# Kernel optimization log

Measured on AMD Instinct MI355X. Metric: run time of the kernel, lower is better.

## Reference

```python
import jax, jax.numpy as jnp
import numpy as np
from jax import lax

TS = 64.0  # timestep_ in the original module


def get_spikes(x, th):
    # Integrate-and-fire with reset-by-subtraction (catCuda.getSpikes),
    # batched over all channels with per-channel thresholds.
    # x: [N,C,H,W,T], th: [C]
    thb = th[None, :, None, None]
    xT = jnp.moveaxis(x, -1, 0)  # [T,N,C,H,W]

    def step(v, xt):
        v = v + xt
        s = (v >= thb).astype(x.dtype)
        return v - s * thb, s

    _, sT = lax.scan(step, jnp.zeros_like(xT[0]), xT)
    return jnp.moveaxis(sT, 0, -1)  # [N,C,H,W,T]


def conv2d(x, w, b, pad):
    out = lax.conv_general_dilated(x, w, (1, 1), [(pad, pad), (pad, pad)],
                                   dimension_numbers=('NCHW', 'OIHW', 'NCHW'))
    return out + b[None, :, None, None]


def snn_conv(x, w, b, pad):
    # per-timestep 2D conv on [N,C,H,W,T]: fold T into batch
    N, C, H, W, T = x.shape
    xt = jnp.moveaxis(x, -1, 1).reshape(N * T, C, H, W)
    out = conv2d(xt, w, b, pad)
    Co, Ho, Wo = out.shape[1], out.shape[2], out.shape[3]
    return jnp.moveaxis(out.reshape(N, T, Co, Ho, Wo), 1, -1)


def avgpool2(y):
    N, C, H, W = y.shape
    return y.reshape(N, C, H // 2, 2, W // 2, 2).mean(axis=(3, 5))


def snn_pool(x):
    N, C, H, W, T = x.shape
    return x.reshape(N, C, H // 2, 2, W // 2, 2, T).mean(axis=(3, 5))


def tt(x5, y4, th):
    # threshold_training_snn: spikes from SNN pre-activation, quantized-clamped
    # ANN activation, and online per-channel threshold update.
    y_new = get_spikes(x5, th)
    y = jnp.clip(jnp.floor(y4 * TS) / TS, 0.0, 1.0)
    mul = x5.shape[0] * x5.shape[2] * x5.shape[3] * x5.shape[4]
    diff = (y.sum(axis=(0, 2, 3)) * TS - y_new.sum(axis=(0, 2, 3, 4))) / mul
    return y_new, y, th - 0.1 * diff


def setup_inputs():
    key = jax.random.key(0)
    ks = jax.random.split(key, 40)
    chans = [(3, 128), (128, 128), (128, 256), (256, 256), (256, 512), (512, 512), (512, 1024)]
    inp = {}
    for idx, (ci, co) in enumerate(chans):
        inp['w%ds' % (idx + 1)] = jax.random.normal(ks[2 * idx], (co, ci, 3, 3), jnp.float32) / np.float32(np.sqrt(ci * 9))
        inp['b%ds' % (idx + 1)] = jnp.zeros((co,), jnp.float32)
        inp['w%da' % (idx + 1)] = jax.random.normal(ks[2 * idx + 1], (co, ci, 3, 3), jnp.float32) / np.float32(np.sqrt(ci * 9))
        inp['b%da' % (idx + 1)] = jnp.zeros((co,), jnp.float32)
    inp['wc'] = jax.random.normal(ks[30], (100, 1024), jnp.float32) / 32.0
    inp['bc'] = jnp.zeros((100,), jnp.float32)
    inp['x'] = jax.random.uniform(ks[31], (4, 3, 32, 32, 64), jnp.float32)
    for name, c in [('threshold_pre_1', 128), ('threshold_pre_2', 128), ('threshold_pre_3', 256),
                    ('threshold_pre_4', 256), ('threshold_pre_5', 512), ('threshold_pre_6', 512),
                    ('threshold_pre_7', 1024), ('p1', 128), ('p2', 256), ('p3', 512), ('p4', 1024)]:
        inp[name] = jnp.ones((c,), jnp.float32)
    return inp


def reference(x, threshold_pre_1, threshold_pre_2, threshold_pre_3, threshold_pre_4,
              threshold_pre_5, threshold_pre_6, threshold_pre_7, p1, p2, p3, p4,
              w1s, b1s, w1a, b1a, w2s, b2s, w2a, b2a, w3s, b3s, w3a, b3a,
              w4s, b4s, w4a, b4a, w5s, b5s, w5a, b5a, w6s, b6s, w6a, b6a,
              w7s, b7s, w7a, b7a, wc, bc):
    x_ = x.sum(axis=-1) / TS
    xs, y, t1 = tt(snn_conv(x, w1s, b1s, 1), conv2d(x_, w1a, b1a, 1), threshold_pre_1)
    xs, y, t2 = tt(snn_conv(xs, w2s, b2s, 1), conv2d(y, w2a, b2a, 1), threshold_pre_2)
    xs, y, q1 = tt(snn_pool(xs), avgpool2(y), p1)
    xs, y, t3 = tt(snn_conv(xs, w3s, b3s, 1), conv2d(y, w3a, b3a, 1), threshold_pre_3)
    xs, y, t4 = tt(snn_conv(xs, w4s, b4s, 1), conv2d(y, w4a, b4a, 1), threshold_pre_4)
    xs, y, q2 = tt(snn_pool(xs), avgpool2(y), p2)
    xs, y, t5 = tt(snn_conv(xs, w5s, b5s, 1), conv2d(y, w5a, b5a, 1), threshold_pre_5)
    xs, y, t6 = tt(snn_conv(xs, w6s, b6s, 1), conv2d(y, w6a, b6a, 1), threshold_pre_6)
    xs, y, q3 = tt(snn_pool(xs), avgpool2(y), p3)
    xs, y, t7 = tt(snn_conv(xs, w7s, b7s, 0), conv2d(y, w7a, b7a, 0), threshold_pre_7)
    xs, y, q4 = tt(snn_pool(xs), avgpool2(y), p4)
    # classifier on [N,1024,1,1,T] spike trains, then sum over time / T
    logits_t = jnp.einsum('nct,oc->not', xs[:, :, 0, 0, :], wc) + bc[None, :, None]
    out = logits_t.sum(axis=-1) / TS
    return (out, t1, t2, t3, t4, t5, t6, t7, q1, q2, q3, q4)
```

## Files before the change

kernel.cpp:

```cpp
#include <hip/hip_runtime.h>
#include <cstdint>
#include <cstddef>


typedef short short8 __attribute__((ext_vector_type(8)));
typedef float floatx4 __attribute__((ext_vector_type(4)));

__device__ __forceinline__ unsigned short f2bf_rne(float f) {
  unsigned u = __float_as_uint(f);
  return (unsigned short)((u + 0x7FFFu + ((u >> 16) & 1u)) >> 16);
}
__device__ __forceinline__ float bf2f(unsigned short h) {
  return __uint_as_float((unsigned)h << 16);
}

__global__ __launch_bounds__(256) void k_wxform(const float* __restrict__ Wsrc,
                                                unsigned short* __restrict__ wt,
                                                int Ci, int Co) {
  const int nch = Ci >> 5;
  const int total = (Co >> 6) * nch * 9 * 4 * 64;
  int idx = blockIdx.x * 256 + threadIdx.x;
  if (idx >= total) return;
  int lane = idx & 63;
  int t2 = idx >> 6;
  int cg = t2 & 3;
  int t3 = t2 >> 2;
  int tap = t3 % 9;
  int t4 = t3 / 9;
  int ch = t4 % nch;
  int cot = t4 / nch;
  int co = cot * 64 + cg * 16 + (lane & 15);
  int cib = ch * 32 + (lane >> 4) * 8;
  short8 vh, vl;
  #pragma unroll
  for (int j = 0; j < 8; ++j) {
    float wv = Wsrc[((size_t)co * Ci + cib + j) * 9 + tap];
    unsigned short h = f2bf_rne(wv);
    vh[j] = (short)h;
    vl[j] = (short)f2bf_rne(wv - bf2f(h));
  }
  size_t base = ((((size_t)cot * nch + ch) * 9 + tap) * 4 + cg) * 1024 + (size_t)lane * 8;
  *(short8*)&wt[base] = vh;
  *(short8*)&wt[base + 512] = vl;
}

__global__ __launch_bounds__(256) void k_wxform1(const float* __restrict__ Wsrc,
                                                 unsigned short* __restrict__ wt) {
  int idx = blockIdx.x * 256 + threadIdx.x;
  if (idx >= 512) return;
  int lane = idx & 63, cg = (idx >> 6) & 3, cot = idx >> 8;
  int co = cot * 64 + cg * 16 + (lane & 15);
  short8 vh, vl;
  #pragma unroll
  for (int e = 0; e < 8; ++e) {
    int k = (lane >> 4) * 8 + e;
    float wv = 0.f;
    if (k < 27) { int tap = k / 3, ci = k - 3 * tap; wv = Wsrc[(co * 3 + ci) * 9 + tap]; }
    unsigned short h = f2bf_rne(wv);
    vh[e] = (short)h;
    vl[e] = (short)f2bf_rne(wv - bf2f(h));
  }
  size_t base = (size_t)cot * 4096 + cg * 1024 + (size_t)lane * 8;
  *(short8*)&wt[base] = vh;
  *(short8*)&wt[base + 512] = vl;
}

__global__ __launch_bounds__(256) void k_tpack(const float* __restrict__ x,
                                               unsigned* __restrict__ XT2) {
  int idx = blockIdx.x * 256 + threadIdx.x;
  int b = idx / 3072;
  int rem = idx - b * 3072;
  int t = b & 63, n = b >> 6;
  float f = x[((size_t)(n * 3072 + rem)) * 64 + t];
  unsigned short h = f2bf_rne(f);
  unsigned short l = f2bf_rne(f - bf2f(h));
  XT2[idx] = (unsigned)h | ((unsigned)l << 16);
}

__global__ __launch_bounds__(256) void k_xbar_pack(const float* __restrict__ x,
                                                   unsigned* __restrict__ xb) {
  int idx = blockIdx.x * 256 + threadIdx.x;
  if (idx >= 12288) return;
  const float* p = x + (size_t)idx * 64;
  float s = 0.f;
  #pragma unroll
  for (int t = 0; t < 64; ++t) s += p[t];
  s *= 0.015625f;
  unsigned short h = f2bf_rne(s);
  unsigned short l = f2bf_rne(s - bf2f(h));
  xb[idx] = (unsigned)h | ((unsigned)l << 16);
}

template <typename T, bool PAD0, int GW, int NPG>
__global__ __launch_bounds__(256, 1) void k_cmfma(
    const T* __restrict__ in, const unsigned short* __restrict__ wt,
    const float* __restrict__ bs, float* __restrict__ out,
    int Ci, int Co, int W, int TRI, int tpi, int NIMG, int nImgValid,
    int nchPer, size_t osplit) {
  constexpr int CW = NPG;
  constexpr int MT = 16 * GW * NPG;
  constexpr int PPXMAX = PAD0 ? (MT / 4) * 16 : 400;
  constexpr int STR = 40;
  __shared__ unsigned short sIn[PPXMAX * STR];
  const int tid = threadIdx.x;
  const int lane = tid & 63;
  const int wv = tid >> 6;
  const int cog = wv / NPG;
  const int pxg = wv % NPG;
  const int cot = blockIdx.x;
  const int mtile = blockIdx.y;
  const int kz = blockIdx.z;
  const int nch = Ci >> 5;
  const int nchA = kz * nchPer, nchB = nchA + nchPer;
  out += (size_t)kz * osplit;
  const int addBias = (kz == 0);

  int img_first, r0 = 0, PPR, PPX;
  if constexpr (PAD0) {
    img_first = mtile * (MT / 4);
    PPR = 16; PPX = (MT / 4) * 16;
  } else {
    img_first = (mtile / tpi) * NIMG;
    r0 = (mtile % tpi) * TRI;
    PPR = (TRI + 2) * (W + 2);
    PPX = NIMG * PPR;
  }
  const int TRW = TRI * W;

  int p0[GW], mimg[GW], mopx[GW];
  #pragma unroll
  for (int g = 0; g < GW; ++g) {
    int m = pxg * (GW * 16) + g * 16 + (lane & 15);
    int limg;
    if constexpr (PAD0) {
      limg = m >> 2;
      int o = m & 3;
      p0[g] = limg * 16 + (o >> 1) * 4 + (o & 1);
      mopx[g] = (o >> 1) * 2 + (o & 1);
    } else {
      limg = m / TRW;
      int rm = m - limg * TRW;
      int r = rm / W, c = rm - r * W;
      p0[g] = limg * PPR + r * (W + 2) + c;
      mopx[g] = (r0 + r) * W + c;
    }
    mimg[g] = img_first + limg;
  }
  int psh[9];
  #pragma unroll
  for (int t = 0; t < 9; ++t) {
    int dh = t / 3, dw = t - dh * 3;
    psh[t] = PAD0 ? (dh * 4 + dw) : (dh * (W + 2) + dw);
  }

  const int HWin = PAD0 ? 16 : W * W;
  int sgofs[2]; bool svalid[2];
  #pragma unroll
  for (int i = 0; i < 2; ++i) {
    int p = tid + i * 256;
    svalid[i] = false; sgofs[i] = 0;
    if (p < PPX) {
      int limg, gpx;
      if constexpr (PAD0) {
        limg = p >> 4; gpx = p & 15;
      } else {
        limg = p / PPR;
        int rem = p - limg * PPR;
        int pr = rem / (W + 2), pc = rem - pr * (W + 2);
        int gr = r0 + pr - 1, gc = pc - 1;
        gpx = (gr >= 0 && gr < W && gc >= 0 && gc < W) ? gr * W + gc : -1;
      }
      int img = img_first + limg;
      if (gpx >= 0 && img < nImgValid) {
        svalid[i] = true;
        sgofs[i] = img * Ci * HWin + gpx;
      }
    }
  }
  const int kb = (lane >> 4) * 8;

  floatx4 acc[CW][GW];
  floatx4 zero = {0.f, 0.f, 0.f, 0.f};
  #pragma unroll
  for (int cw = 0; cw < CW; ++cw)
    #pragma unroll
    for (int g = 0; g < GW; ++g) acc[cw][g] = zero;

  for (int ch = nchA; ch < nchB; ++ch) {
    const int ci0 = ch * 32;
    #pragma unroll
    for (int i = 0; i < 2; ++i) {
      int p = tid + i * 256;
      if (p < PPX) {
        unsigned short* dst = &sIn[p * STR];
        if (svalid[i]) {
          const T* sp = in + sgofs[i] + (size_t)ci0 * HWin;
          #pragma unroll
          for (int j = 0; j < 4; ++j) {
            short8 v;
            #pragma unroll
            for (int e = 0; e < 8; ++e) {
              if constexpr (sizeof(T) == 1)
                v[e] = sp[(size_t)(j * 8 + e) * HWin] ? (short)0x3F80 : (short)0;
              else
                v[e] = (short)f2bf_rne(((const float*)sp)[(size_t)(j * 8 + e) * HWin]);
            }
            *(short8*)&dst[j * 8] = v;
          }
        } else {
          short8 z = {};
          #pragma unroll
          for (int j = 0; j < 4; ++j) *(short8*)&dst[j * 8] = z;
        }
      }
    }
    __syncthreads();
    const unsigned short* wbase = wt + ((size_t)(cot * nch + ch)) * 36864
                                  + (size_t)(cog * CW) * 1024 + (size_t)lane * 8;
    short8 A[2][CW * 2];
    #pragma unroll
    for (int cw = 0; cw < CW; ++cw) {
      A[0][cw * 2 + 0] = *(const short8*)(wbase + cw * 1024);
      A[0][cw * 2 + 1] = *(const short8*)(wbase + cw * 1024 + 512);
    }
    #pragma unroll
    for (int t = 0; t < 9; ++t) {
      const int cur = t & 1;
      if (t < 8) {
        const unsigned short* wp = wbase + (size_t)(t + 1) * 4096;
        #pragma unroll
        for (int cw = 0; cw < CW; ++cw) {
          A[cur ^ 1][cw * 2 + 0] = *(const short8*)(wp + cw * 1024);
          A[cur ^ 1][cw * 2 + 1] = *(const short8*)(wp + cw * 1024 + 512);
        }
      }
      short8 b[GW];
      #pragma unroll
      for (int g = 0; g < GW; ++g)
        b[g] = *(const short8*)&sIn[(p0[g] + psh[t]) * STR + kb];
      #pragma unroll
      for (int cw = 0; cw < CW; ++cw) {
        #pragma unroll
        for (int g = 0; g < GW; ++g) {
          acc[cw][g] = __builtin_amdgcn_mfma_f32_16x16x32_bf16(A[cur][cw * 2 + 0], b[g], acc[cw][g], 0, 0, 0);
          acc[cw][g] = __builtin_amdgcn_mfma_f32_16x16x32_bf16(A[cur][cw * 2 + 1], b[g], acc[cw][g], 0, 0, 0);
        }
      }
    }
    __syncthreads();
  }
  const int HWout = PAD0 ? 4 : W * W;
  #pragma unroll
  for (int g = 0; g < GW; ++g) {
    if (mimg[g] >= nImgValid) continue;
    #pragma unroll
    for (int cw = 0; cw < CW; ++cw) {
      #pragma unroll
      for (int i2 = 0; i2 < 4; ++i2) {
        int co = cot * 64 + (cog * CW + cw) * 16 + (lane >> 4) * 4 + i2;
        float bv = addBias ? bs[co] : 0.f;
        out[((size_t)mimg[g] * Co + co) * HWout + mopx[g]] = acc[cw][g][i2] + bv;
      }
    }
  }
}

__global__ __launch_bounds__(256, 1) void k_l1(const unsigned* __restrict__ xin,
                                               const unsigned short* __restrict__ wt,
                                               const float* __restrict__ bs,
                                               float* __restrict__ out,
                                               int nImgValid) {
  __shared__ unsigned short sIn[256 * 72];
  const int tid = threadIdx.x, lane = tid & 63, wv = tid >> 6;
  const int cot = blockIdx.x, mtile = blockIdx.y;
  const int img = mtile >> 2;
  const int r0 = (mtile & 3) * 8;
  {
    int m = tid;
    int r = r0 + (m >> 5), c = m & 31;
    const unsigned* ip = xin + (size_t)img * 3072;
    unsigned v[9][3];
    bool iv = (img < nImgValid);
    #pragma unroll
    for (int dh = 0; dh < 3; ++dh) {
      #pragma unroll
      for (int dw = 0; dw < 3; ++dw) {
        int rr = r + dh - 1, cc = c + dw - 1;
        bool ok = iv && rr >= 0 && rr < 32 && cc >= 0 && cc < 32;
        #pragma unroll
        for (int ci = 0; ci < 3; ++ci)
          v[dh * 3 + dw][ci] = ok ? ip[ci * 1024 + rr * 32 + cc] : 0u;
      }
    }
    #pragma unroll
    for (int j = 0; j < 4; ++j) {
      short8 vh, vl;
      #pragma unroll
      for (int e = 0; e < 8; ++e) {
        int k = j * 8 + e;
        unsigned u = (k < 27) ? v[k / 3][k - 3 * (k / 3)] : 0u;
        vh[e] = (short)(u & 0xFFFFu);
        vl[e] = (short)(u >> 16);
      }
      *(short8*)&sIn[m * 72 + j * 8] = vh;
      *(short8*)&sIn[m * 72 + 32 + j * 8] = vl;
    }
  }
  __syncthreads();
  const int kb = (lane >> 4) * 8;
  const unsigned short* wb = wt + (size_t)cot * 4096 + (size_t)lane * 8;
  short8 Af[8];
  #pragma unroll
  for (int f = 0; f < 8; ++f)
    Af[f] = *(const short8*)(wb + (f >> 1) * 1024 + (f & 1) * 512);
  floatx4 acc[4][4];
  floatx4 zero = {0.f, 0.f, 0.f, 0.f};
  #pragma unroll
  for (int cg = 0; cg < 4; ++cg)
    #pragma unroll
    for (int g = 0; g < 4; ++g) acc[cg][g] = zero;
  short8 bh[4], bl[4];
  #pragma unroll
  for (int g = 0; g < 4; ++g) {
    int m = wv * 64 + g * 16 + (lane & 15);
    bh[g] = *(const short8*)&sIn[m * 72 + kb];
    bl[g] = *(const short8*)&sIn[m * 72 + 32 + kb];
  }
  #pragma unroll
  for (int cg = 0; cg < 4; ++cg) {
    #pragma unroll
    for (int g = 0; g < 4; ++g) {
      acc[cg][g] = __builtin_amdgcn_mfma_f32_16x16x32_bf16(Af[cg * 2 + 0], bh[g], acc[cg][g], 0, 0, 0);
      acc[cg][g] = __builtin_amdgcn_mfma_f32_16x16x32_bf16(Af[cg * 2 + 0], bl[g], acc[cg][g], 0, 0, 0);
      acc[cg][g] = __builtin_amdgcn_mfma_f32_16x16x32_bf16(Af[cg * 2 + 1], bh[g], acc[cg][g], 0, 0, 0);
    }
  }
  if (img >= nImgValid) return;
  #pragma unroll
  for (int g = 0; g < 4; ++g) {
    int mbase = wv * 64 + g * 16 + (lane & 15);
    int px = (r0 + (mbase >> 5)) * 32 + (mbase & 31);
    #pragma unroll
    for (int cg = 0; cg < 4; ++cg) {
      #pragma unroll
      for (int i2 = 0; i2 < 4; ++i2) {
        int co = cot * 64 + cg * 16 + (lane >> 4) * 4 + i2;
        out[((size_t)img * 128 + co) * 1024 + px] = acc[cg][g][i2] + bs[co];
      }
    }
  }
}

__global__ __launch_bounds__(256) void k_if(const float* __restrict__ X,
                                            uint8_t* __restrict__ Sp,
                                            const float* __restrict__ th,
                                            float* __restrict__ ssum,
                                            int C, int HW,
                                            int nparts, size_t pstride) {
  const int CHW = C * HW;
  int idx = blockIdx.x * 256 + threadIdx.x;
  if (idx >= CHW) return;
  int c = idx / HW;
  const float thv = th[c];
  size_t base = (size_t)blockIdx.y * 64 * CHW + idx;
  const float* p = X + base;
  uint8_t* q = Sp + base;
  float v = 0.f, ss = 0.f;
  #pragma unroll
  for (int t = 0; t < 64; ++t) {
    const float* pt = p + (size_t)t * CHW;
    float xv = pt[0];
    for (int u = 1; u < nparts; ++u) xv += pt[(size_t)u * pstride];
    v += xv;
    float s = (v >= thv) ? 1.f : 0.f;
    v -= s * thv;
    q[(size_t)t * CHW] = (uint8_t)s;
    ss += s;
  }
  if ((HW & 63) == 0) {
    for (int off = 32; off >= 1; off >>= 1) ss += __shfl_down(ss, off);
    if ((threadIdx.x & 63) == 0) atomicAdd(&ssum[c], ss);
  } else {
    atomicAdd(&ssum[c], ss);
  }
}

__global__ __launch_bounds__(256) void k_ifpool(const uint8_t* __restrict__ Sin,
                                                uint8_t* __restrict__ Sp,
                                                const float* __restrict__ th,
                                                float* __restrict__ ssum,
                                                float* __restrict__ Sout,
                                                int C, int H) {
  const int Ho = H >> 1, HWo = Ho * Ho;
  const int CHWo = C * HWo;
  int idx = blockIdx.x * 256 + threadIdx.x;
  if (idx >= CHWo) return;
  int c = idx / HWo;
  int rem = idx - c * HWo;
  int ho = rem / Ho, wo = rem - ho * Ho;
  const float thv = th[c];
  const size_t istep = (size_t)C * H * H;
  const size_t ib = ((size_t)(blockIdx.y * 64) * C + c) * (H * H) + (2 * ho) * H + 2 * wo;
  uint8_t* q = Sp + (size_t)blockIdx.y * 64 * CHWo + idx;
  float v = 0.f, ss = 0.f;
  #pragma unroll
  for (int t = 0; t < 64; ++t) {
    const uint8_t* pp = Sin + ib + (size_t)t * istep;
    float xv = 0.25f * ((float)pp[0] + (float)pp[1] + (float)pp[H] + (float)pp[H + 1]);
    v += xv;
    float s = (v >= thv) ? 1.f : 0.f;
    v -= s * thv;
    q[(size_t)t * CHWo] = (uint8_t)s;
    ss += s;
  }
  if (Sout && HWo == 1) Sout[blockIdx.y * C + c] = ss;
  if ((HWo & 63) == 0) {
    for (int off = 32; off >= 1; off >>= 1) ss += __shfl_down(ss, off);
    if ((threadIdx.x & 63) == 0) atomicAdd(&ssum[c], ss);
  } else {
    atomicAdd(&ssum[c], ss);
  }
}

__global__ __launch_bounds__(256) void k_ttypool(const float* __restrict__ yin,
                                                 float* __restrict__ yout,
                                                 float* __restrict__ ysum,
                                                 int C, int H) {
  const int Ho = H >> 1, HWo = Ho * Ho;
  int idx = blockIdx.x * 256 + threadIdx.x;
  if (idx >= 4 * C * HWo) return;
  int rem = idx % (C * HWo);
  int c = rem / HWo;
  int r2 = rem - c * HWo;
  int ho = r2 / Ho, wo = r2 - ho * Ho;
  int img = idx / (C * HWo);
  size_t base = (((size_t)img * C + c) * H + 2 * ho) * H + 2 * wo;
  float xv = 0.25f * (yin[base] + yin[base + 1] + yin[base + H] + yin[base + H + 1]);
  float v = floorf(xv * 64.f) * 0.015625f;
  v = fminf(fmaxf(v, 0.f), 1.f);
  yout[idx] = v;
  if ((HWo & 63) == 0) {
    for (int off = 32; off >= 1; off >>= 1) v += __shfl_down(v, off);
    if ((threadIdx.x & 63) == 0) atomicAdd(&ysum[c], v);
  } else {
    atomicAdd(&ysum[c], v);
  }
}

__global__ __launch_bounds__(256) void k_tty(const float* __restrict__ y4,
                                             float* __restrict__ yout,
                                             float* __restrict__ ysum,
                                             int C, int HW,
                                             int nparts, int pstride) {
  int idx = blockIdx.x * 256 + threadIdx.x;
  if (idx >= 4 * C * HW) return;
  int rem = idx % (C * HW);
  int c = rem / HW;
  float xv = 0.f;
  for (int p = 0; p < nparts; ++p) xv += y4[idx + (size_t)p * pstride];
  float v = floorf(xv * 64.f) * 0.015625f;
  v = fminf(fmaxf(v, 0.f), 1.f);
  yout[idx] = v;
  if ((HW & 63) == 0) {
    for (int off = 32; off >= 1; off >>= 1) v += __shfl_down(v, off);
    if ((threadIdx.x & 63) == 0) atomicAdd(&ysum[c], v);
  } else {
    atomicAdd(&ysum[c], v);
  }
}

__global__ void k_thr(const float* __restrict__ thin,
                      const float* __restrict__ ssum,
                      const float* __restrict__ ysum,
                      float* __restrict__ dst, int C, float invmul) {
  int c = blockIdx.x * 256 + threadIdx.x;
  if (c >= C) return;
  float diff = (ysum[c] * 64.f - ssum[c]) * invmul;
  dst[c] = thin[c] - 0.1f * diff;
}

__global__ void k_cls(const float* __restrict__ S, const float* __restrict__ wc,
                      const float* __restrict__ bcp, float* __restrict__ out) {
  int idx = blockIdx.x * 256 + threadIdx.x;
  if (idx >= 400) return;
  int n = idx / 100, o = idx - (idx / 100) * 100;
  const float* sp = S + n * 1024;
  const float* wp = wc + o * 1024;
  float acc = 0.f;
  for (int c = 0; c < 1024; ++c) acc += wp[c] * sp[c];
  out[idx] = acc * 0.015625f + bcp[o];
}

extern "C" void kernel_launch(void* const* d_in, const int* in_sizes, int n_in,
                              void* d_out_v, int out_size, void* d_ws, size_t ws_size,
                              hipStream_t stream) {
  const float *Ws[7], *Bs[7], *Wa[7], *Ba[7];
  for (int i = 0; i < 7; ++i) {
    Ws[i] = (const float*)d_in[i * 4 + 0];
    Bs[i] = (const float*)d_in[i * 4 + 1];
    Wa[i] = (const float*)d_in[i * 4 + 2];
    Ba[i] = (const float*)d_in[i * 4 + 3];
  }
  const float* wc = (const float*)d_in[28];
  const float* bc = (const float*)d_in[29];
  const float* x  = (const float*)d_in[30];
  const float* TH[7];
  for (int i = 0; i < 7; ++i) TH[i] = (const float*)d_in[31 + i];
  const float* P[4];
  for (int i = 0; i < 4; ++i) P[i] = (const float*)d_in[38 + i];
  float* out = (float*)d_out_v;

  float* w = (float*)d_ws;
  const size_t RF = 8536064;
  float* Rb = w;
  size_t off = RF;
  float* xbar = w + off; off += 12288;
  float* yA   = w + off; off += 524288;
  float* yB   = w + off; off += 524288;
  float* y4   = w + off; off += 524288;
  float* S    = w + off; off += 4096;
  float* sums = w + off; off += 11 * 2048;
  uint8_t* SA = (uint8_t*)(w + off);
  uint8_t* SB = SA + 33554432;
  size_t total_bytes = off * sizeof(float) + (size_t)2 * 33554432;
  if (ws_size < total_bytes) return;
  unsigned short* WT = (unsigned short*)Rb;
  unsigned* XT2 = (unsigned*)SB;
  unsigned* xbar2 = (unsigned*)xbar;

  hipMemsetAsync(sums, 0, 11 * 2048 * sizeof(float), stream);
  k_tpack<<<3072, 256, 0, stream>>>(x, XT2);
  k_xbar_pack<<<48, 256, 0, stream>>>(x, xbar2);

  int stage = 0;

  {
    float* CF = Rb + 4096;
    float* ss = sums; float* ys = ss + 1024;
    k_wxform1<<<2, 256, 0, stream>>>(Ws[0], WT);
    for (int c = 0; c < 4; ++c) {
      k_l1<<<dim3(2, 256), 256, 0, stream>>>(XT2 + (size_t)c * 64 * 3072, WT, Bs[0], CF, 64);
      k_if<<<dim3(512, 1), 256, 0, stream>>>(CF, SA + (size_t)c * 64 * 131072,
                                             TH[0], ss, 128, 1024, 1, 0);
    }
    k_wxform1<<<2, 256, 0, stream>>>(Wa[0], WT);
    k_l1<<<dim3(2, 16), 256, 0, stream>>>(xbar2, WT, Ba[0], y4, 4);
    k_tty<<<2048, 256, 0, stream>>>(y4, yA, ys, 128, 1024, 1, 0);
    k_thr<<<1, 256, 0, stream>>>(TH[0], ss, ys, out + 400, 128, 1.0f / (4.f * 1024.f * 64.f));
    ++stage;
  }

  auto mfma_layer = [&](const uint8_t* inS, uint8_t* outS, const float* inY, float* outY,
                        int li, int Ci, int Co, int W, int TRI, int tpi, int NIMG,
                        int chunkImgs, int kzn, float* CF1,
                        int aTRI, int atpi, int akz,
                        const float* thin, int outoff) {
    const int HW = W * W;
    const int CHWo = Co * HW;
    const int nch = Ci >> 5;
    float* ss = sums + stage * 2048; float* ys = ss + 1024;
    float* CF = Rb + (size_t)Co * Ci * 9;
    size_t osplit = (kzn == 2) ? (size_t)(CF1 - CF) : 0;
    int xgrid = ((Co / 64) * nch * 9 * 4 * 64 + 255) / 256;
    k_wxform<<<xgrid, 256, 0, stream>>>(Ws[li], WT, Ci, Co);
    int nchk = 256 / chunkImgs;
    int mt = (chunkImgs / NIMG) * tpi;
    for (int c = 0; c < nchk; ++c) {
      k_cmfma<uint8_t, false, 8, 2><<<dim3(Co / 64, mt, kzn), 256, 0, stream>>>(
          inS + (size_t)c * chunkImgs * Ci * HW, WT, Bs[li], CF,
          Ci, Co, W, TRI, tpi, NIMG, chunkImgs, nch / kzn, osplit);
      k_if<<<dim3((CHWo + 255) / 256, chunkImgs / 64), 256, 0, stream>>>(
          CF, outS + (size_t)c * chunkImgs * CHWo, thin, ss, Co, HW, kzn, osplit);
    }
    k_wxform<<<xgrid, 256, 0, stream>>>(Wa[li], WT, Ci, Co);
    int aosplit = 4 * CHWo;
    k_cmfma<float, false, 4, 1><<<dim3(Co / 64, 4 * atpi, akz), 256, 0, stream>>>(
        inY, WT, Ba[li], y4, Ci, Co, W, aTRI, atpi, 1, 4, nch / akz, (size_t)aosplit);
    k_tty<<<(4 * CHWo + 255) / 256, 256, 0, stream>>>(y4, outY, ys, Co, HW, akz, aosplit);
    k_thr<<<(Co + 255) / 256, 256, 0, stream>>>(thin, ss, ys, out + outoff, Co,
                                                1.0f / (4.f * HW * 64.f));
    ++stage;
  };

  auto pool_stage = [&](const uint8_t* inS, uint8_t* outS, const float* inY, float* outY,
                        int C, int H, const float* pthr, int outoff, float* Sout) {
    const int Ho = H / 2, HWo = Ho * Ho;
    const int CHWo = C * HWo;
    float* ss = sums + stage * 2048; float* ys = ss + 1024;
    k_ifpool<<<dim3((CHWo + 255) / 256, 4), 256, 0, stream>>>(inS, outS, pthr, ss, Sout, C, H);
    k_ttypool<<<(4 * CHWo + 255) / 256, 256, 0, stream>>>(inY, outY, ys, C, H);
    k_thr<<<(C + 255) / 256, 256, 0, stream>>>(pthr, ss, ys, out + outoff, C,
                                               1.0f / (4.f * HWo * 64.f));
    ++stage;
  };

  mfma_layer(SA, SB, yA, yB, 1, 128, 128, 32, 8, 4, 1, 64, 1, nullptr,
             2, 16, 1, TH[1], 528);
  pool_stage(SB, SA, yB, yA, 128, 32, P[0], 3216, nullptr);
  mfma_layer(SA, SB, yA, yB, 2, 128, 256, 16, 16, 1, 1, 64, 2,
             (float*)(SB + 16777216), 4, 4, 2, TH[2], 656);
  mfma_layer(SB, SA, yB, yA, 3, 256, 256, 16, 16, 1, 1, 64, 2,
             (float*)(SA + 16777216), 4, 4, 2, TH[3], 912);
  pool_stage(SA, SB, yA, yB, 256, 16, P[1], 3344, nullptr);
  mfma_layer(SB, SA, yB, yA, 4, 256, 512, 8, 8, 1, 4, 128, 2,
             (float*)(SA + 8388608), 8, 1, 4, TH[4], 1168);
  mfma_layer(SA, SB, yA, yB, 5, 512, 512, 8, 8, 1, 4, 128, 2,
             (float*)(SB + 8388608), 8, 1, 4, TH[5], 1680);
  pool_stage(SB, SA, yB, yA, 512, 8, P[2], 3600, nullptr);
  {
    float* ss = sums + stage * 2048; float* ys = ss + 1024;
    float* CF = (float*)(SA + 4194304);
    const size_t osplit = 1048576;
    int xgrid = (16 * 16 * 9 * 4 * 64 + 255) / 256;
    k_wxform<<<xgrid, 256, 0, stream>>>(Ws[6], WT, 512, 1024);
    k_cmfma<uint8_t, true, 8, 1><<<dim3(16, 8, 4), 256, 0, stream>>>(
        SA, WT, Bs[6], CF, 512, 1024, 4, 0, 1, 0, 256, 4, osplit);
    k_if<<<dim3(16, 4), 256, 0, stream>>>(CF, SB, TH[6], ss, 1024, 4, 4, osplit);
    k_wxform<<<xgrid, 256, 0, stream>>>(Wa[6], WT, 512, 1024);
    k_cmfma<float, true, 4, 1><<<dim3(16, 1, 8), 256, 0, stream>>>(
        yA, WT, Ba[6], y4, 512, 1024, 4, 0, 1, 0, 4, 2, 16384);
    k_tty<<<64, 256, 0, stream>>>(y4, yB, ys, 1024, 4, 8, 16384);
    k_thr<<<4, 256, 0, stream>>>(TH[6], ss, ys, out + 2192, 1024, 1.0f / 1024.f);
    ++stage;
  }
  pool_stage(SB, SA, yB, yA, 1024, 2, P[3], 4112, S);
  k_cls<<<2, 256, 0, stream>>>(S, wc, bc, out);
}
```

Measured before the change: 1.801 ms.

## Double-buffer LDS input staging in conv MFMA kernel with register prefetch

For the padded-conv variant, the shared-memory input tile is double-buffered. The next channel chunk's global loads are issued into registers before the MFMA tap loop and written to the alternate buffer afterwards, which removes one barrier per chunk and hides global load latency behind compute. The cost is double the LDS footprint and up to 64 extra registers per thread for the prefetch, which could cause spills given launch_bounds(256,1) and the existing accumulator pressure.

```diff
diff --git a/kernel.cpp b/kernel.cpp
--- a/kernel.cpp
+++ b/kernel.cpp
@@ -101,7 +101,8 @@
   constexpr int MT = 16 * GW * NPG;
   constexpr int PPXMAX = PAD0 ? (MT / 4) * 16 : 400;
   constexpr int STR = 40;
-  __shared__ unsigned short sIn[PPXMAX * STR];
+  constexpr int NBUF = PAD0 ? 1 : 2;
+  __shared__ unsigned short sIn[NBUF][PPXMAX * STR];
   const int tid = threadIdx.x;
   const int lane = tid & 63;
   const int wv = tid >> 6;
@@ -179,20 +180,13 @@
   }
   const int kb = (lane >> 4) * 8;
 
-  floatx4 acc[CW][GW];
-  floatx4 zero = {0.f, 0.f, 0.f, 0.f};
-  #pragma unroll
-  for (int cw = 0; cw < CW; ++cw)
-    #pragma unroll
-    for (int g = 0; g < GW; ++g) acc[cw][g] = zero;
-
-  for (int ch = nchA; ch < nchB; ++ch) {
+  auto stage_direct = [&](int ch, unsigned short* buf) {
     const int ci0 = ch * 32;
     #pragma unroll
     for (int i = 0; i < 2; ++i) {
       int p = tid + i * 256;
       if (p < PPX) {
-        unsigned short* dst = &sIn[p * STR];
+        unsigned short* dst = &buf[p * STR];
         if (svalid[i]) {
           const T* sp = in + sgofs[i] + (size_t)ci0 * HWin;
           #pragma unroll
@@ -214,7 +208,16 @@
         }
       }
     }
-    __syncthreads();
+  };
+
+  floatx4 acc[CW][GW];
+  floatx4 zero = {0.f, 0.f, 0.f, 0.f};
+  #pragma unroll
+  for (int cw = 0; cw < CW; ++cw)
+    #pragma unroll
+    for (int g = 0; g < GW; ++g) acc[cw][g] = zero;
+
+  auto run_taps = [&](const unsigned short* buf, int ch) {
     const unsigned short* wbase = wt + ((size_t)(cot * nch + ch)) * 36864
                                   + (size_t)(cog * CW) * 1024 + (size_t)lane * 8;
     short8 A[2][CW * 2];
@@ -237,7 +240,7 @@
       short8 b[GW];
       #pragma unroll
       for (int g = 0; g < GW; ++g)
-        b[g] = *(const short8*)&sIn[(p0[g] + psh[t]) * STR + kb];
+        b[g] = *(const short8*)&buf[(p0[g] + psh[t]) * STR + kb];
       #pragma unroll
       for (int cw = 0; cw < CW; ++cw) {
         #pragma unroll
@@ -247,7 +250,67 @@
         }
       }
     }
+  };
+
+  if constexpr (NBUF == 1) {
+    for (int ch = nchA; ch < nchB; ++ch) {
+      stage_direct(ch, sIn[0]);
+      __syncthreads();
+      run_taps(sIn[0], ch);
+      __syncthreads();
+    }
+  } else {
+    stage_direct(nchA, sIn[0]);
     __syncthreads();
+    for (int ch = nchA; ch < nchB; ++ch) {
+      const int cur = (ch - nchA) & 1;
+      const bool pre = (ch + 1 < nchB);
+      uint8_t ru[2][32];
+      float rf[2][32];
+      if (pre) {
+        const int ci0n = (ch + 1) * 32;
+        #pragma unroll
+        for (int i = 0; i < 2; ++i) {
+          if (tid + i * 256 < PPX && svalid[i]) {
+            const T* sp = in + sgofs[i] + (size_t)ci0n * HWin;
+            #pragma unroll
+            for (int k = 0; k < 32; ++k) {
+              if constexpr (sizeof(T) == 1) ru[i][k] = sp[(size_t)k * HWin];
+              else rf[i][k] = ((const float*)sp)[(size_t)k * HWin];
+            }
+          }
+        }
+      }
+      run_taps(sIn[cur], ch);
+      if (pre) {
+        #pragma unroll
+        for (int i = 0; i < 2; ++i) {
+          int p = tid + i * 256;
+          if (p < PPX) {
+            unsigned short* dst = &sIn[cur ^ 1][p * STR];
+            if (svalid[i]) {
+              #pragma unroll
+              for (int j = 0; j < 4; ++j) {
+                short8 v;
+                #pragma unroll
+                for (int e = 0; e < 8; ++e) {
+                  if constexpr (sizeof(T) == 1)
+                    v[e] = ru[i][j * 8 + e] ? (short)0x3F80 : (short)0;
+                  else
+                    v[e] = (short)f2bf_rne(rf[i][j * 8 + e]);
+                }
+                *(short8*)&dst[j * 8] = v;
+              }
+            } else {
+              short8 z = {};
+              #pragma unroll
+              for (int j = 0; j < 4; ++j) *(short8*)&dst[j * 8] = z;
+            }
+          }
+        }
+      }
+      __syncthreads();
+    }
   }
   const int HWout = PAD0 ? 4 : W * W;
   #pragma unroll
```

Result: slower. 2.356 ms (+30.8%).
